# Kernel tuning notes

Measured on AMD Instinct MI355X. Metric: run time of the kernel, lower is better.

The kernel has to match this reference:

```python
import jax, jax.numpy as jnp
import numpy as np


def setup_inputs() -> dict:
    key = jax.random.key(0)
    k1, k2 = jax.random.split(key)
    B, Lc, Lm, D = 8, 2048, 2048, 128
    context = jax.random.normal(k1, (B, Lc, D), dtype=jnp.float32)
    main = jax.random.normal(k2, (B, Lm, D), dtype=jnp.float32)
    return {"context": context, "main": main}


def reference(context, main):
    # weights[b,c,m] = sum_d context[b,c,d] * main[b,m,d]   (Keras dot axes=[2,2])
    weights = jnp.einsum("bcd,bmd->bcm", context, main)
    # K.softmax default axis=-1: normalize over the main-length axis m
    weights = jax.nn.softmax(weights, axis=-1)
    # dot([weights, context], axes=1): contract axis 1 (c) of both -> (B, Lm, D)
    weighted = jnp.einsum("bcm,bcd->bmd", weights, context)
    return main - weighted
```

## Files before the change

kernel.cpp:

```cpp
#include <hip/hip_runtime.h>


#define BATCH 8
#define L_SEQ 2048
#define DD 128
#define SHIFT 40.0f
#define LDA 136

typedef __attribute__((ext_vector_type(8))) short bf16x8;
typedef __attribute__((ext_vector_type(4))) short bf16x4;
typedef __attribute__((ext_vector_type(4))) float f32x4;

__device__ __forceinline__ short f2bf(float f) {
    unsigned u = __builtin_bit_cast(unsigned, f);
    return (short)((u + 0x8000u) >> 16);
}

__device__ __forceinline__ void gl2lds16(const short* g, short* l) {
    __builtin_amdgcn_global_load_lds(
        (const __attribute__((address_space(1))) unsigned int*)g,
        (__attribute__((address_space(3))) unsigned int*)l, 16, 0, 0);
}

template <int NT>
__device__ __forceinline__ void stage_tile(short* __restrict__ dst,
                                           const float* __restrict__ src,
                                           int nelts, int t) {
    for (int base = 0; base < nelts; base += NT * 8) {
        int flat = base + t * 8;
        const float4* p = (const float4*)(src + flat);
        float4 v0 = p[0];
        float4 v1 = p[1];
        bf16x8 s;
        s[0] = f2bf(v0.x); s[1] = f2bf(v0.y); s[2] = f2bf(v0.z); s[3] = f2bf(v0.w);
        s[4] = f2bf(v1.x); s[5] = f2bf(v1.y); s[6] = f2bf(v1.z); s[7] = f2bf(v1.w);
        int row = flat >> 7;
        int col = flat & 127;
        *(bf16x8*)&dst[row * LDA + col] = s;
    }
}

__global__ __launch_bounds__(256) void zero_kernel(float* __restrict__ p, int n) {
    int i = blockIdx.x * 256 + threadIdx.x;
    if (i < n) p[i] = 0.0f;
}


__global__ __launch_bounds__(256) void convert_kernel(const float* __restrict__ ctx,
                                                      const float* __restrict__ mn,
                                                      short* __restrict__ Cbf,
                                                      short* __restrict__ Mbf,
                                                      float* __restrict__ Lg) {
    int tid = blockIdx.x * 256 + threadIdx.x;
    if (tid < BATCH * L_SEQ) Lg[tid] = 0.0f;
    const int half = BATCH * L_SEQ * DD / 8;
    int id = tid;
    const float* src;
    short* dst;
    if (id < half) { src = ctx; dst = Cbf; }
    else           { id -= half; src = mn; dst = Mbf; }
    int row = id >> 4;
    int lc = id & 15;
    const float4* p = (const float4*)(src + ((size_t)row << 7) + lc * 8);
    float4 v0 = p[0];
    float4 v1 = p[1];
    bf16x8 s;
    s[0] = f2bf(v0.x); s[1] = f2bf(v0.y); s[2] = f2bf(v0.z); s[3] = f2bf(v0.w);
    s[4] = f2bf(v1.x); s[5] = f2bf(v1.y); s[6] = f2bf(v1.z); s[7] = f2bf(v1.w);
    int pc = (lc & 8) | ((lc ^ row) & 7);
    *(bf16x8*)&dst[((size_t)row << 7) + pc * 8] = s;
}

__global__ __launch_bounds__(256, 2) void stats_kernel(const short* __restrict__ Cbf,
                                                       const short* __restrict__ Mbf,
                                                       float* __restrict__ Lg,
                                                       short* __restrict__ Eg) {
    __shared__ short Cs[128 * 128];
    __shared__ short Ms[2][64 * 128];

    int bid = blockIdx.x;
    int mc = bid & 3;
    int ct = (bid >> 2) & 15;
    int b  = bid >> 6;
    int t = threadIdx.x;
    int w = t >> 6;
    int l = t & 63;
    int a15 = l & 15;
    int q = l >> 4;
    int h = a15 & 7;
    int cw = (w & 1) * 64;
    int mw = (w >> 1) * 32;

    {
        const short* gC = Cbf + ((size_t)(b * L_SEQ + ct * 128)) * DD;
        const short* gM = Mbf + ((size_t)(b * L_SEQ + mc * 512)) * DD;
        #pragma unroll
        for (int ii = 0; ii < 8; ++ii) {
            int inst = w * 8 + ii;
            gl2lds16(gC + inst * 512 + l * 8, Cs + inst * 512);
        }
        #pragma unroll
        for (int ii = 0; ii < 4; ++ii) {
            int inst = w * 4 + ii;
            gl2lds16(gM + inst * 512 + l * 8, Ms[0] + inst * 512);
        }
    }

    __syncthreads();

    {
        const short* gM = Mbf + ((size_t)(b * L_SEQ + mc * 512 + 64)) * DD;
        #pragma unroll
        for (int ii = 0; ii < 4; ++ii) {
            int inst = w * 4 + ii;
            gl2lds16(gM + inst * 512 + l * 8, Ms[1] + inst * 512);
        }
    }

    bf16x8 af[4][4];
    #pragma unroll
    for (int ks = 0; ks < 4; ++ks) {
        int aoff = ((ks * 4 + q) ^ h) * 8;
        #pragma unroll
        for (int i = 0; i < 4; ++i)
            af[ks][i] = *(const bf16x8*)&Cs[(cw + i * 16 + a15) * 128 + aoff];
    }

    float ls[4][4] = {};

    for (int ms = 0; ms < 8; ++ms) {
        int bp = ms & 1;
        if (ms > 0) {
            __syncthreads();
            if (ms < 7) {
                const short* gM = Mbf + ((size_t)(b * L_SEQ + mc * 512 + (ms + 1) * 64)) * DD;
                #pragma unroll
                for (int ii = 0; ii < 4; ++ii) {
                    int inst = w * 4 + ii;
                    gl2lds16(gM + inst * 512 + l * 8, Ms[bp ^ 1] + inst * 512);
                }
            }
        }

        f32x4 acc[4][2];
        #pragma unroll
        for (int i = 0; i < 4; ++i)
            #pragma unroll
            for (int j = 0; j < 2; ++j) {
                f32x4 z = {0.f, 0.f, 0.f, 0.f};
                acc[i][j] = z;
            }
        #pragma unroll
        for (int ks = 0; ks < 4; ++ks) {
            int aoff = ((ks * 4 + q) ^ h) * 8;
            bf16x8 bv[2];
            #pragma unroll
            for (int j = 0; j < 2; ++j)
                bv[j] = *(const bf16x8*)&Ms[bp][(mw + j * 16 + a15) * 128 + aoff];
            #pragma unroll
            for (int i = 0; i < 4; ++i)
                #pragma unroll
                for (int j = 0; j < 2; ++j)
                    acc[i][j] = __builtin_amdgcn_mfma_f32_16x16x32_bf16(af[ks][i], bv[j], acc[i][j], 0, 0, 0);
        }

        #pragma unroll
        for (int j = 0; j < 2; ++j) {
            int m = mc * 512 + ms * 64 + mw + j * 16 + a15;
            size_t rowb = ((size_t)(b * L_SEQ + m)) * L_SEQ;
            #pragma unroll
            for (int i = 0; i < 4; ++i) {
                bf16x4 pk;
                #pragma unroll
                for (int r = 0; r < 4; ++r) {
                    float e = __expf(acc[i][j][r] - SHIFT);
                    ls[i][r] += e;
                    pk[r] = f2bf(e);
                }
                int cq = ct * 128 + cw + i * 16 + q * 4;
                int chunk = cq >> 3;
                int pcc = (chunk & ~7) | ((chunk ^ m) & 7);
                *(bf16x4*)&Eg[rowb + pcc * 8 + (cq & 7)] = pk;
            }
        }
    }

    #pragma unroll
    for (int i = 0; i < 4; ++i)
        #pragma unroll
        for (int r = 0; r < 4; ++r) {
            float v = ls[i][r];
            v += __shfl_xor(v, 1);
            v += __shfl_xor(v, 2);
            v += __shfl_xor(v, 4);
            v += __shfl_xor(v, 8);
            ls[i][r] = v;
        }
    if (a15 == 0) {
        #pragma unroll
        for (int i = 0; i < 4; ++i) {
            int c = ct * 128 + cw + i * 16 + q * 4;
            #pragma unroll
            for (int r = 0; r < 4; ++r)
                atomicAdd(&Lg[(size_t)b * L_SEQ + c + r], ls[i][r]);
        }
    }
}

__global__ __launch_bounds__(256) void prep_kernel(const float* __restrict__ ctx,
                                                   const float* __restrict__ Lg,
                                                   short* __restrict__ CtL) {
    __shared__ short Ts[128 * LDA];
    __shared__ float invLs[128];

    int b = blockIdx.x >> 4;
    int cc = blockIdx.x & 15;
    int t = threadIdx.x;

    if (t < 128) invLs[t] = 1.0f / Lg[(size_t)b * L_SEQ + cc * 128 + t];
    __syncthreads();

    const float* src = ctx + ((size_t)(b * L_SEQ + cc * 128)) * DD;
    #pragma unroll
    for (int i = 0; i < 8; ++i) {
        int flat = i * 2048 + t * 8;
        int r = flat >> 7;
        int c = flat & 127;
        const float4* p = (const float4*)(src + flat);
        float4 v0 = p[0];
        float4 v1 = p[1];
        float il = invLs[r];
        bf16x8 s;
        s[0] = f2bf(v0.x * il); s[1] = f2bf(v0.y * il); s[2] = f2bf(v0.z * il); s[3] = f2bf(v0.w * il);
        s[4] = f2bf(v1.x * il); s[5] = f2bf(v1.y * il); s[6] = f2bf(v1.z * il); s[7] = f2bf(v1.w * il);
        *(bf16x8*)&Ts[r * LDA + c] = s;
    }
    __syncthreads();

    int d = t >> 1;
    int ch = (t & 1) * 64;
    int key = d & 7;
    #pragma unroll
    for (int i = 0; i < 8; ++i) {
        int c = ch + i * 8;
        bf16x8 v;
        #pragma unroll
        for (int j = 0; j < 8; ++j) v[j] = Ts[(c + j) * LDA + d];
        int pc = cc * 16 + (ch >> 3) + (i ^ key);
        *(bf16x8*)&CtL[((size_t)(b * DD + d)) * L_SEQ + pc * 8] = v;
    }
}

__global__ __launch_bounds__(256, 2) void attend_kernel(const short* __restrict__ Eg,
                                                        const short* __restrict__ CtL,
                                                        const float* __restrict__ mn,
                                                        float* __restrict__ out) {
    __shared__ short Et2[2][32 * 128];
    __shared__ short Ct2[2][128 * 128];

    int bid = blockIdx.x;
    int mtile = bid & 63;
    int b = bid >> 6;
    int m0 = mtile * 32;
    int t = threadIdx.x;
    int w = t >> 6;
    int l = t & 63;
    int a15 = l & 15;
    int q = l >> 4;
    int h = a15 & 7;
    int lcc = l & 15;

    f32x4 acc[2][2] = {{{0.f,0.f,0.f,0.f},{0.f,0.f,0.f,0.f}},
                       {{0.f,0.f,0.f,0.f},{0.f,0.f,0.f,0.f}}};

    #pragma unroll
    for (int ii = 0; ii < 2; ++ii) {
        int inst = w * 2 + ii;
        gl2lds16(Eg + ((size_t)(b * L_SEQ + m0 + inst * 4 + q)) * L_SEQ + lcc * 8,
                 &Et2[0][inst * 512]);
    }
    #pragma unroll
    for (int ii = 0; ii < 8; ++ii) {
        int inst = w * 8 + ii;
        gl2lds16(CtL + ((size_t)(b * DD + inst * 4 + q)) * L_SEQ + lcc * 8,
                 &Ct2[0][inst * 512]);
    }

    for (int cs = 0; cs < 16; ++cs) {
        int bp = cs & 1;
        __syncthreads();

        if (cs < 15) {
            int c0 = (cs + 1) * 128;
            #pragma unroll
            for (int ii = 0; ii < 2; ++ii) {
                int inst = w * 2 + ii;
                gl2lds16(Eg + ((size_t)(b * L_SEQ + m0 + inst * 4 + q)) * L_SEQ + c0 + lcc * 8,
                         &Et2[bp ^ 1][inst * 512]);
            }
            #pragma unroll
            for (int ii = 0; ii < 8; ++ii) {
                int inst = w * 8 + ii;
                gl2lds16(CtL + ((size_t)(b * DD + inst * 4 + q)) * L_SEQ + c0 + lcc * 8,
                         &Ct2[bp ^ 1][inst * 512]);
            }
        }

        const short* EtB = Et2[bp];
        const short* CtB = Ct2[bp];
        #pragma unroll
        for (int ks = 0; ks < 4; ++ks) {
            int aoff = ((ks * 4 + q) ^ h) * 8;
            bf16x8 a0 = *(const bf16x8*)&EtB[a15 * 128 + aoff];
            bf16x8 a1 = *(const bf16x8*)&EtB[(16 + a15) * 128 + aoff];
            bf16x8 b0 = *(const bf16x8*)&CtB[((w * 2 + 0) * 16 + a15) * 128 + aoff];
            bf16x8 b1 = *(const bf16x8*)&CtB[((w * 2 + 1) * 16 + a15) * 128 + aoff];
            acc[0][0] = __builtin_amdgcn_mfma_f32_16x16x32_bf16(a0, b0, acc[0][0], 0, 0, 0);
            acc[0][1] = __builtin_amdgcn_mfma_f32_16x16x32_bf16(a0, b1, acc[0][1], 0, 0, 0);
            acc[1][0] = __builtin_amdgcn_mfma_f32_16x16x32_bf16(a1, b0, acc[1][0], 0, 0, 0);
            acc[1][1] = __builtin_amdgcn_mfma_f32_16x16x32_bf16(a1, b1, acc[1][1], 0, 0, 0);
        }
    }

    #pragma unroll
    for (int mg = 0; mg < 2; ++mg) {
        #pragma unroll
        for (int g = 0; g < 2; ++g) {
            int d = (w * 2 + g) * 16 + a15;
            #pragma unroll
            for (int r = 0; r < 4; ++r) {
                int m = m0 + mg * 16 + q * 4 + r;
                size_t idx = ((size_t)(b * L_SEQ + m)) * DD + d;
                out[idx] = mn[idx] - acc[mg][g][r];
            }
        }
    }
}


__global__ __launch_bounds__(256, 4) void stats_fb(const float* __restrict__ ctx,
                                                   const float* __restrict__ mn,
                                                   float* __restrict__ Lg) {
    __shared__ short Cs[64 * LDA];
    __shared__ short Ms[64 * LDA];

    int bid = blockIdx.x;
    int mc = bid & 3;
    int ct = (bid >> 2) & 31;
    int b  = bid >> 7;
    int t = threadIdx.x;
    int w = t >> 6;
    int l = t & 63;
    int a15 = l & 15;
    int q = l >> 4;

    stage_tile<256>(Cs, ctx + ((size_t)b * L_SEQ + ct * 64) * DD, 64 * DD, t);

    float ls[4] = {0.f, 0.f, 0.f, 0.f};
    for (int mt = 0; mt < 8; ++mt) {
        __syncthreads();
        int m0 = (mc * 8 + mt) * 64;
        stage_tile<256>(Ms, mn + ((size_t)b * L_SEQ + m0) * DD, 64 * DD, t);
        __syncthreads();

        f32x4 acc[4] = {{0.f,0.f,0.f,0.f},{0.f,0.f,0.f,0.f},{0.f,0.f,0.f,0.f},{0.f,0.f,0.f,0.f}};
        #pragma unroll
        for (int ks = 0; ks < 4; ++ks) {
            int k0 = ks * 32 + q * 8;
            bf16x8 a = *(const bf16x8*)&Cs[(w * 16 + a15) * LDA + k0];
            #pragma unroll
            for (int g = 0; g < 4; ++g) {
                bf16x8 bb = *(const bf16x8*)&Ms[(g * 16 + a15) * LDA + k0];
                acc[g] = __builtin_amdgcn_mfma_f32_16x16x32_bf16(a, bb, acc[g], 0, 0, 0);
            }
        }
        #pragma unroll
        for (int g = 0; g < 4; ++g)
            #pragma unroll
            for (int r = 0; r < 4; ++r)
                ls[r] += __expf(acc[g][r] - SHIFT);
    }

    #pragma unroll
    for (int r = 0; r < 4; ++r) {
        float v = ls[r];
        v += __shfl_xor(v, 1);
        v += __shfl_xor(v, 2);
        v += __shfl_xor(v, 4);
        v += __shfl_xor(v, 8);
        ls[r] = v;
    }
    if (a15 == 0) {
        int c = ct * 64 + w * 16 + q * 4;
        #pragma unroll
        for (int r = 0; r < 4; ++r)
            atomicAdd(&Lg[(size_t)b * L_SEQ + c + r], ls[r]);
    }
}

__global__ __launch_bounds__(1024, 4) void attend_fb(const float* __restrict__ ctx,
                                                     const float* __restrict__ mn,
                                                     const float* __restrict__ Lg,
                                                     float* __restrict__ out) {
    __shared__ short Mt[64 * LDA];
    __shared__ short Cs[128 * LDA];
    __shared__ short Ct[128 * LDA];
    __shared__ short Ps[64 * LDA];
    __shared__ float invLs[128];

    int bid = blockIdx.x;
    int mtile = bid & 31;
    int b = bid >> 5;
    int m0 = mtile * 64;
    int t = threadIdx.x;
    int w = t >> 6;
    int l = t & 63;
    int a15 = l & 15;
    int q = l >> 4;
    int mg = w & 3;
    int pg = w >> 2;

    stage_tile<1024>(Mt, mn + ((size_t)b * L_SEQ + m0) * DD, 64 * DD, t);

    f32x4 oacc[2] = {{0.f,0.f,0.f,0.f},{0.f,0.f,0.f,0.f}};

    for (int cs = 0; cs < 16; ++cs) {
        int c0 = cs * 128;
        __syncthreads();
        stage_tile<1024>(Cs, ctx + ((size_t)b * L_SEQ + c0) * DD, 128 * DD, t);
        if (t < 128) invLs[t] = 1.0f / Lg[(size_t)b * L_SEQ + c0 + t];
        __syncthreads();

        {
            int cc = t & 127;
            int d0 = (t >> 7) * 16;
            #pragma unroll
            for (int hh = 0; hh < 2; ++hh) {
                bf16x8 v = *(const bf16x8*)&Cs[cc * LDA + d0 + hh * 8];
                #pragma unroll
                for (int j = 0; j < 8; ++j)
                    Ct[(d0 + hh * 8 + j) * LDA + cc] = v[j];
            }
        }

        f32x4 sacc[2] = {{0.f,0.f,0.f,0.f},{0.f,0.f,0.f,0.f}};
        #pragma unroll
        for (int ks = 0; ks < 4; ++ks) {
            int k0 = ks * 32 + q * 8;
            bf16x8 a = *(const bf16x8*)&Mt[(mg * 16 + a15) * LDA + k0];
            #pragma unroll
            for (int g = 0; g < 2; ++g) {
                bf16x8 bb = *(const bf16x8*)&Cs[((pg * 2 + g) * 16 + a15) * LDA + k0];
                sacc[g] = __builtin_amdgcn_mfma_f32_16x16x32_bf16(a, bb, sacc[g], 0, 0, 0);
            }
        }
        #pragma unroll
        for (int g = 0; g < 2; ++g) {
            int cl = (pg * 2 + g) * 16 + a15;
            float il = invLs[cl];
            #pragma unroll
            for (int r = 0; r < 4; ++r) {
                float p = __expf(sacc[g][r] - SHIFT) * il;
                Ps[(mg * 16 + q * 4 + r) * LDA + cl] = f2bf(p);
            }
        }
        __syncthreads();

        #pragma unroll
        for (int ks = 0; ks < 4; ++ks) {
            int k0 = ks * 32 + q * 8;
            bf16x8 a = *(const bf16x8*)&Ps[(mg * 16 + a15) * LDA + k0];
            #pragma unroll
            for (int g = 0; g < 2; ++g) {
                bf16x8 bb = *(const bf16x8*)&Ct[((pg * 2 + g) * 16 + a15) * LDA + k0];
                oacc[g] = __builtin_amdgcn_mfma_f32_16x16x32_bf16(a, bb, oacc[g], 0, 0, 0);
            }
        }
    }

    #pragma unroll
    for (int g = 0; g < 2; ++g) {
        int dl = (pg * 2 + g) * 16 + a15;
        #pragma unroll
        for (int r = 0; r < 4; ++r) {
            int ml = mg * 16 + q * 4 + r;
            size_t idx = ((size_t)b * L_SEQ + m0 + ml) * DD + dl;
            out[idx] = mn[idx] - oacc[g][r];
        }
    }
}


extern "C" void kernel_launch(void* const* d_in, const int* in_sizes, int n_in,
                              void* d_out, int out_size, void* d_ws, size_t ws_size,
                              hipStream_t stream) {
    const float* ctx = (const float*)d_in[0];
    const float* mn  = (const float*)d_in[1];
    float* out = (float*)d_out;

    const size_t LG_BYTES = (size_t)BATCH * L_SEQ * sizeof(float);
    const size_t BF_BYTES = (size_t)BATCH * L_SEQ * DD * sizeof(short);
    const size_t E_BYTES  = (size_t)BATCH * L_SEQ * L_SEQ * sizeof(short);
    const size_t NEED = LG_BYTES + 3 * BF_BYTES + E_BYTES;

    float* Lg = (float*)d_ws;

    if (ws_size >= NEED) {
        short* Cbf = (short*)((char*)d_ws + LG_BYTES);
        short* Mbf = (short*)((char*)d_ws + LG_BYTES + BF_BYTES);
        short* CtL = (short*)((char*)d_ws + LG_BYTES + 2 * BF_BYTES);
        short* Eg  = (short*)((char*)d_ws + LG_BYTES + 3 * BF_BYTES);
        convert_kernel<<<2048, 256, 0, stream>>>(ctx, mn, Cbf, Mbf, Lg);
        stats_kernel<<<BATCH * 16 * 4, 256, 0, stream>>>(Cbf, Mbf, Lg, Eg);
        prep_kernel<<<BATCH * 16, 256, 0, stream>>>(ctx, Lg, CtL);
        attend_kernel<<<BATCH * 64, 256, 0, stream>>>(Eg, CtL, mn, out);
    } else {
        int nL = BATCH * L_SEQ;
        zero_kernel<<<(nL + 255) / 256, 256, 0, stream>>>(Lg, nL);
        stats_fb<<<BATCH * 32 * 4, 256, 0, stream>>>(ctx, mn, Lg);
        attend_fb<<<BATCH * 32, 1024, 0, stream>>>(ctx, mn, Lg, out);
    }
}
```

Measured before the change: 115.3 us.

## Fuse four-phase pipeline into one cooperative kernel with grid syncs

```diff
diff --git a/kernel.cpp b/kernel.cpp
--- a/kernel.cpp
+++ b/kernel.cpp
@@ -1,4 +1,7 @@
 #include <hip/hip_runtime.h>
+#include <hip/hip_cooperative_groups.h>
+
+namespace cg = cooperative_groups;
 
 
 #define BATCH 8
@@ -14,6 +17,10 @@
 __device__ __forceinline__ short f2bf(float f) {
     unsigned u = __builtin_bit_cast(unsigned, f);
     return (short)((u + 0x8000u) >> 16);
+}
+__device__ __forceinline__ float bf2f(short s) {
+    unsigned u = ((unsigned)(unsigned short)s) << 16;
+    return __builtin_bit_cast(float, u);
 }
 
 __device__ __forceinline__ void gl2lds16(const short* g, short* l) {
@@ -46,43 +53,46 @@
 }
 
 
-__global__ __launch_bounds__(256) void convert_kernel(const float* __restrict__ ctx,
-                                                      const float* __restrict__ mn,
-                                                      short* __restrict__ Cbf,
-                                                      short* __restrict__ Mbf,
-                                                      float* __restrict__ Lg) {
-    int tid = blockIdx.x * 256 + threadIdx.x;
-    if (tid < BATCH * L_SEQ) Lg[tid] = 0.0f;
+__device__ __forceinline__ void convert_phase(int gtid,
+                                              const float* __restrict__ ctx,
+                                              const float* __restrict__ mn,
+                                              short* __restrict__ Cbf,
+                                              short* __restrict__ Mbf,
+                                              float* __restrict__ Lg) {
+    if (gtid < BATCH * L_SEQ) Lg[gtid] = 0.0f;
     const int half = BATCH * L_SEQ * DD / 8;
-    int id = tid;
-    const float* src;
-    short* dst;
-    if (id < half) { src = ctx; dst = Cbf; }
-    else           { id -= half; src = mn; dst = Mbf; }
-    int row = id >> 4;
-    int lc = id & 15;
-    const float4* p = (const float4*)(src + ((size_t)row << 7) + lc * 8);
-    float4 v0 = p[0];
-    float4 v1 = p[1];
-    bf16x8 s;
-    s[0] = f2bf(v0.x); s[1] = f2bf(v0.y); s[2] = f2bf(v0.z); s[3] = f2bf(v0.w);
-    s[4] = f2bf(v1.x); s[5] = f2bf(v1.y); s[6] = f2bf(v1.z); s[7] = f2bf(v1.w);
-    int pc = (lc & 8) | ((lc ^ row) & 7);
-    *(bf16x8*)&dst[((size_t)row << 7) + pc * 8] = s;
-}
-
-__global__ __launch_bounds__(256, 2) void stats_kernel(const short* __restrict__ Cbf,
-                                                       const short* __restrict__ Mbf,
-                                                       float* __restrict__ Lg,
-                                                       short* __restrict__ Eg) {
-    __shared__ short Cs[128 * 128];
-    __shared__ short Ms[2][64 * 128];
-
-    int bid = blockIdx.x;
+    #pragma unroll
+    for (int k = 0; k < 4; ++k) {
+        int id = gtid + k * (512 * 256);
+        const float* src;
+        short* dst;
+        int iid = id;
+        if (iid < half) { src = ctx; dst = Cbf; }
+        else            { iid -= half; src = mn; dst = Mbf; }
+        int row = iid >> 4;
+        int lc = iid & 15;
+        const float4* p = (const float4*)(src + ((size_t)row << 7) + lc * 8);
+        float4 v0 = p[0];
+        float4 v1 = p[1];
+        bf16x8 s;
+        s[0] = f2bf(v0.x); s[1] = f2bf(v0.y); s[2] = f2bf(v0.z); s[3] = f2bf(v0.w);
+        s[4] = f2bf(v1.x); s[5] = f2bf(v1.y); s[6] = f2bf(v1.z); s[7] = f2bf(v1.w);
+        int pc = (lc & 8) | ((lc ^ row) & 7);
+        *(bf16x8*)&dst[((size_t)row << 7) + pc * 8] = s;
+    }
+}
+
+__device__ __forceinline__ void stats_phase(char* smemc, int bid, int t,
+                                            const short* __restrict__ Cbf,
+                                            const short* __restrict__ Mbf,
+                                            float* __restrict__ Lg,
+                                            short* __restrict__ Eg) {
+    short* Cs = (short*)smemc;
+    short* MsB[2] = {(short*)(smemc + 32768), (short*)(smemc + 49152)};
+
     int mc = bid & 3;
     int ct = (bid >> 2) & 15;
     int b  = bid >> 6;
-    int t = threadIdx.x;
     int w = t >> 6;
     int l = t & 63;
     int a15 = l & 15;
@@ -102,7 +112,7 @@
         #pragma unroll
         for (int ii = 0; ii < 4; ++ii) {
             int inst = w * 4 + ii;
-            gl2lds16(gM + inst * 512 + l * 8, Ms[0] + inst * 512);
+            gl2lds16(gM + inst * 512 + l * 8, MsB[0] + inst * 512);
         }
     }
 
@@ -113,7 +123,7 @@
         #pragma unroll
         for (int ii = 0; ii < 4; ++ii) {
             int inst = w * 4 + ii;
-            gl2lds16(gM + inst * 512 + l * 8, Ms[1] + inst * 512);
+            gl2lds16(gM + inst * 512 + l * 8, MsB[1] + inst * 512);
         }
     }
 
@@ -137,7 +147,7 @@
                 #pragma unroll
                 for (int ii = 0; ii < 4; ++ii) {
                     int inst = w * 4 + ii;
-                    gl2lds16(gM + inst * 512 + l * 8, Ms[bp ^ 1] + inst * 512);
+                    gl2lds16(gM + inst * 512 + l * 8, MsB[bp ^ 1] + inst * 512);
                 }
             }
         }
@@ -156,7 +166,7 @@
             bf16x8 bv[2];
             #pragma unroll
             for (int j = 0; j < 2; ++j)
-                bv[j] = *(const bf16x8*)&Ms[bp][(mw + j * 16 + a15) * 128 + aoff];
+                bv[j] = *(const bf16x8*)&MsB[bp][(mw + j * 16 + a15) * 128 + aoff];
             #pragma unroll
             for (int i = 0; i < 4; ++i)
                 #pragma unroll
@@ -207,62 +217,60 @@
     }
 }
 
-__global__ __launch_bounds__(256) void prep_kernel(const float* __restrict__ ctx,
-                                                   const float* __restrict__ Lg,
-                                                   short* __restrict__ CtL) {
-    __shared__ short Ts[128 * LDA];
-    __shared__ float invLs[128];
-
-    int b = blockIdx.x >> 4;
-    int cc = blockIdx.x & 15;
-    int t = threadIdx.x;
+__device__ __forceinline__ void prep_phase(char* smemc, int bid, int t,
+                                           const short* __restrict__ Cbf,
+                                           const float* __restrict__ Lg,
+                                           short* __restrict__ CtL) {
+    short* Ts = (short*)smemc;
+    float* invLs = (float*)(smemc + 34816);
+
+    int b  = bid >> 6;
+    int cc = (bid >> 2) & 15;
+    int dq = bid & 3;
 
     if (t < 128) invLs[t] = 1.0f / Lg[(size_t)b * L_SEQ + cc * 128 + t];
     __syncthreads();
 
-    const float* src = ctx + ((size_t)(b * L_SEQ + cc * 128)) * DD;
-    #pragma unroll
-    for (int i = 0; i < 8; ++i) {
-        int flat = i * 2048 + t * 8;
-        int r = flat >> 7;
-        int c = flat & 127;
-        const float4* p = (const float4*)(src + flat);
-        float4 v0 = p[0];
-        float4 v1 = p[1];
+    #pragma unroll
+    for (int it = 0; it < 8; ++it) {
+        int cid = it * 256 + t;
+        int r = cid >> 4;
+        int lcs = cid & 15;
+        int lc = (lcs & 8) | ((lcs ^ r) & 7);
+        bf16x8 v = *(const bf16x8*)&Cbf[((size_t)(b * L_SEQ + cc * 128 + r)) * DD + lcs * 8];
         float il = invLs[r];
-        bf16x8 s;
-        s[0] = f2bf(v0.x * il); s[1] = f2bf(v0.y * il); s[2] = f2bf(v0.z * il); s[3] = f2bf(v0.w * il);
-        s[4] = f2bf(v1.x * il); s[5] = f2bf(v1.y * il); s[6] = f2bf(v1.z * il); s[7] = f2bf(v1.w * il);
-        *(bf16x8*)&Ts[r * LDA + c] = s;
+        bf16x8 sv;
+        #pragma unroll
+        for (int j = 0; j < 8; ++j) sv[j] = f2bf(bf2f(v[j]) * il);
+        *(bf16x8*)&Ts[r * LDA + lc * 8] = sv;
     }
     __syncthreads();
 
-    int d = t >> 1;
-    int ch = (t & 1) * 64;
+    int d = dq * 32 + (t >> 3);
     int key = d & 7;
     #pragma unroll
-    for (int i = 0; i < 8; ++i) {
-        int c = ch + i * 8;
+    for (int it = 0; it < 2; ++it) {
+        int chIdx = (t & 7) + 8 * it;
+        int c = chIdx * 8;
         bf16x8 v;
         #pragma unroll
         for (int j = 0; j < 8; ++j) v[j] = Ts[(c + j) * LDA + d];
-        int pc = cc * 16 + (ch >> 3) + (i ^ key);
+        int pc = cc * 16 + (chIdx & 8) + ((chIdx ^ key) & 7);
         *(bf16x8*)&CtL[((size_t)(b * DD + d)) * L_SEQ + pc * 8] = v;
     }
 }
 
-__global__ __launch_bounds__(256, 2) void attend_kernel(const short* __restrict__ Eg,
-                                                        const short* __restrict__ CtL,
-                                                        const float* __restrict__ mn,
-                                                        float* __restrict__ out) {
-    __shared__ short Et2[2][32 * 128];
-    __shared__ short Ct2[2][128 * 128];
-
-    int bid = blockIdx.x;
+__device__ __forceinline__ void attend_phase(char* smemc, int bid, int t,
+                                             const short* __restrict__ Eg,
+                                             const short* __restrict__ CtL,
+                                             const float* __restrict__ mn,
+                                             float* __restrict__ out) {
+    short* EtB2[2] = {(short*)smemc, (short*)(smemc + 8192)};
+    short* CtB2[2] = {(short*)(smemc + 16384), (short*)(smemc + 49152)};
+
     int mtile = bid & 63;
     int b = bid >> 6;
     int m0 = mtile * 32;
-    int t = threadIdx.x;
     int w = t >> 6;
     int l = t & 63;
     int a15 = l & 15;
@@ -277,13 +285,13 @@
     for (int ii = 0; ii < 2; ++ii) {
         int inst = w * 2 + ii;
         gl2lds16(Eg + ((size_t)(b * L_SEQ + m0 + inst * 4 + q)) * L_SEQ + lcc * 8,
-                 &Et2[0][inst * 512]);
+                 EtB2[0] + inst * 512);
     }
     #pragma unroll
     for (int ii = 0; ii < 8; ++ii) {
         int inst = w * 8 + ii;
         gl2lds16(CtL + ((size_t)(b * DD + inst * 4 + q)) * L_SEQ + lcc * 8,
-                 &Ct2[0][inst * 512]);
+                 CtB2[0] + inst * 512);
     }
 
     for (int cs = 0; cs < 16; ++cs) {
@@ -296,18 +304,18 @@
             for (int ii = 0; ii < 2; ++ii) {
                 int inst = w * 2 + ii;
                 gl2lds16(Eg + ((size_t)(b * L_SEQ + m0 + inst * 4 + q)) * L_SEQ + c0 + lcc * 8,
-                         &Et2[bp ^ 1][inst * 512]);
+                         EtB2[bp ^ 1] + inst * 512);
             }
             #pragma unroll
             for (int ii = 0; ii < 8; ++ii) {
                 int inst = w * 8 + ii;
                 gl2lds16(CtL + ((size_t)(b * DD + inst * 4 + q)) * L_SEQ + c0 + lcc * 8,
-                         &Ct2[bp ^ 1][inst * 512]);
-            }
-        }
-
-        const short* EtB = Et2[bp];
-        const short* CtB = Ct2[bp];
+                         CtB2[bp ^ 1] + inst * 512);
+            }
+        }
+
+        const short* EtB = EtB2[bp];
+        const short* CtB = CtB2[bp];
         #pragma unroll
         for (int ks = 0; ks < 4; ++ks) {
             int aoff = ((ks * 4 + q) ^ h) * 8;
@@ -335,6 +343,60 @@
             }
         }
     }
+}
+
+
+__global__ __launch_bounds__(256, 2) void fused_kernel(const float* __restrict__ ctx,
+                                                       const float* __restrict__ mn,
+                                                       float* __restrict__ out,
+                                                       short* __restrict__ Cbf,
+                                                       short* __restrict__ Mbf,
+                                                       short* __restrict__ CtL,
+                                                       short* __restrict__ Eg,
+                                                       float* __restrict__ Lg) {
+    __shared__ __align__(16) char smem[81920];
+    cg::grid_group grid = cg::this_grid();
+    int bid = blockIdx.x;
+    int t = threadIdx.x;
+
+    convert_phase(bid * 256 + t, ctx, mn, Cbf, Mbf, Lg);
+    grid.sync();
+    stats_phase(smem, bid, t, Cbf, Mbf, Lg, Eg);
+    grid.sync();
+    prep_phase(smem, bid, t, Cbf, Lg, CtL);
+    grid.sync();
+    attend_phase(smem, bid, t, Eg, CtL, mn, out);
+}
+
+__global__ __launch_bounds__(256, 2) void convert_kernel(const float* __restrict__ ctx,
+                                                         const float* __restrict__ mn,
+                                                         short* __restrict__ Cbf,
+                                                         short* __restrict__ Mbf,
+                                                         float* __restrict__ Lg) {
+    convert_phase(blockIdx.x * 256 + threadIdx.x, ctx, mn, Cbf, Mbf, Lg);
+}
+
+__global__ __launch_bounds__(256, 2) void stats_kernel(const short* __restrict__ Cbf,
+                                                       const short* __restrict__ Mbf,
+                                                       float* __restrict__ Lg,
+                                                       short* __restrict__ Eg) {
+    __shared__ __align__(16) char smem[65536];
+    stats_phase(smem, blockIdx.x, threadIdx.x, Cbf, Mbf, Lg, Eg);
+}
+
+__global__ __launch_bounds__(256, 2) void prep_kernel(const short* __restrict__ Cbf,
+                                                      const float* __restrict__ Lg,
+                                                      short* __restrict__ CtL) {
+    __shared__ __align__(16) char smem[35328];
+    prep_phase(smem, blockIdx.x, threadIdx.x, Cbf, Lg, CtL);
+}
+
+__global__ __launch_bounds__(256, 2) void attend_kernel(const short* __restrict__ Eg,
+                                                        const short* __restrict__ CtL,
+                                                        const float* __restrict__ mn,
+                                                        float* __restrict__ out) {
+    __shared__ __align__(16) char smem[81920];
+    attend_phase(smem, blockIdx.x, threadIdx.x, Eg, CtL, mn, out);
 }
 
 
@@ -510,10 +572,25 @@
         short* Mbf = (short*)((char*)d_ws + LG_BYTES + BF_BYTES);
         short* CtL = (short*)((char*)d_ws + LG_BYTES + 2 * BF_BYTES);
         short* Eg  = (short*)((char*)d_ws + LG_BYTES + 3 * BF_BYTES);
-        convert_kernel<<<2048, 256, 0, stream>>>(ctx, mn, Cbf, Mbf, Lg);
-        stats_kernel<<<BATCH * 16 * 4, 256, 0, stream>>>(Cbf, Mbf, Lg, Eg);
-        prep_kernel<<<BATCH * 16, 256, 0, stream>>>(ctx, Lg, CtL);
-        attend_kernel<<<BATCH * 64, 256, 0, stream>>>(Eg, CtL, mn, out);
+
+        int dev = 0;
+        (void)hipGetDevice(&dev);
+        int coop = 0;
+        (void)hipDeviceGetAttribute(&coop, hipDeviceAttributeCooperativeLaunch, dev);
+
+        hipError_t err = hipErrorUnknown;
+        if (coop) {
+            void* kargs[] = {(void*)&ctx, (void*)&mn, (void*)&out, (void*)&Cbf,
+                             (void*)&Mbf, (void*)&CtL, (void*)&Eg, (void*)&Lg};
+            err = hipLaunchCooperativeKernel((const void*)fused_kernel, dim3(512),
+                                             dim3(256), kargs, 0, stream);
+        }
+        if (err != hipSuccess) {
+            convert_kernel<<<512, 256, 0, stream>>>(ctx, mn, Cbf, Mbf, Lg);
+            stats_kernel<<<512, 256, 0, stream>>>(Cbf, Mbf, Lg, Eg);
+            prep_kernel<<<512, 256, 0, stream>>>(Cbf, Lg, CtL);
+            attend_kernel<<<512, 256, 0, stream>>>(Eg, CtL, mn, out);
+        }
     } else {
         int nL = BATCH * L_SEQ;
         zero_kernel<<<(nL + 255) / 256, 256, 0, stream>>>(Lg, nL);
```

Measured after the change: 300.3 us. 2.61x slower.
